# Kernel optimization log

Measured on AMD Instinct MI355X. Metric: run time of the kernel, lower is better.

The kernel has to match this reference:

```python
import jax, jax.numpy as jnp
import numpy as np

B, S, MSL, MQL = 512, 20, 32, 16
E, H, HQ = 32, 32, 32
V, A = 10000, 1000
D = H + S  # per-object feature dim (hidden + one-hot tag) = 52
G = 256


def _lstm_last_h(x, Wih, Whh, bih, bhh):
    # x: [N, T, E]; torch LSTM gate order i,f,g,o; returns final hidden [N, H]
    n, t, _ = x.shape
    h_dim = Whh.shape[1]
    xp = jnp.einsum('nte,ge->ntg', x, Wih) + bih + bhh  # precompute input projection

    def step(carry, xt):
        h, c = carry
        gates = xt + h @ Whh.T
        i, f, g, o = jnp.split(gates, 4, axis=-1)
        c = jax.nn.sigmoid(f) * c + jax.nn.sigmoid(i) * jnp.tanh(g)
        h = jax.nn.sigmoid(o) * jnp.tanh(c)
        return (h, c), None

    init = (jnp.zeros((n, h_dim), x.dtype), jnp.zeros((n, h_dim), x.dtype))
    (h, _), _ = jax.lax.scan(step, init, xp.transpose(1, 0, 2))
    return h


def setup_inputs() -> dict:
    key = jax.random.key(0)
    ks = jax.random.split(key, 24)
    nrm = lambda k, shp, std=0.1: (jax.random.normal(k, shp) * std).astype(jnp.float32)
    inp = {
        'story': jax.random.randint(ks[0], (B, S, MSL), 0, V),
        'question': jax.random.randint(ks[1], (B, MQL), 0, V),
        'emb': nrm(ks[2], (V, E)),
        's_Wih': nrm(ks[3], (4 * H, E)),
        's_Whh': nrm(ks[4], (4 * H, H)),
        's_bih': jnp.zeros((4 * H,), jnp.float32),
        's_bhh': jnp.zeros((4 * H,), jnp.float32),
        'q_Wih': nrm(ks[5], (4 * HQ, E)),
        'q_Whh': nrm(ks[6], (4 * HQ, HQ)),
        'q_bih': jnp.zeros((4 * HQ,), jnp.float32),
        'q_bhh': jnp.zeros((4 * HQ,), jnp.float32),
        'g1_w': nrm(ks[7], (G, 2 * D + HQ)), 'g1_b': jnp.zeros((G,), jnp.float32),
        'g2_w': nrm(ks[8], (G, G)), 'g2_b': jnp.zeros((G,), jnp.float32),
        'g3_w': nrm(ks[9], (G, G)), 'g3_b': jnp.zeros((G,), jnp.float32),
        'g4_w': nrm(ks[10], (G, G)), 'g4_b': jnp.zeros((G,), jnp.float32),
        'f1_w': nrm(ks[11], (G, G)), 'f1_b': jnp.zeros((G,), jnp.float32),
        'f2_w': nrm(ks[12], (512, G)), 'f2_b': jnp.zeros((512,), jnp.float32),
        'f3_w': nrm(ks[13], (A, 512)), 'f3_b': jnp.zeros((A,), jnp.float32),
    }
    return inp


def reference(story, question, emb, s_Wih, s_Whh, s_bih, s_bhh,
              q_Wih, q_Whh, q_bih, q_bhh,
              g1_w, g1_b, g2_w, g2_b, g3_w, g3_b, g4_w, g4_b,
              f1_w, f1_b, f2_w, f2_b, f3_w, f3_b):
    bsz = story.shape[0]
    # story encoding: LSTM over each sentence, take final hidden state
    s_emb = emb[story].reshape(bsz * S, MSL, E)
    s_state = _lstm_last_h(s_emb, s_Wih, s_Whh, s_bih, s_bhh).reshape(bsz, S, H)
    # append one-hot position tags -> story objects [B, S, H+S]
    tags = jnp.broadcast_to(jnp.eye(S, dtype=s_state.dtype), (bsz, S, S))
    obj = jnp.concatenate([s_state, tags], axis=2)
    # question encoding
    q_state = _lstm_last_h(emb[question], q_Wih, q_Whh, q_bih, q_bhh)  # [B, HQ]
    # g_theta over all S*S pairs: g1(cat(o_i, o_j, q)) split into three projections
    Wa, Wb, Wq = g1_w[:, :D], g1_w[:, D:2 * D], g1_w[:, 2 * D:]
    pi = jnp.einsum('bsd,gd->bsg', obj, Wa)   # object-as-first projection
    pj = jnp.einsum('bsd,gd->bsg', obj, Wb)   # object-as-second projection
    pq = q_state @ Wq.T                        # [B, G]
    x = jax.nn.relu(pi[:, :, None, :] + pj[:, None, :, :] + pq[:, None, None, :] + g1_b)  # [B,S,S,G]
    x = jax.nn.relu(jnp.einsum('bijg,hg->bijh', x, g2_w) + g2_b)
    x = jax.nn.relu(jnp.einsum('bijg,hg->bijh', x, g3_w) + g3_b)
    x = jax.nn.relu(jnp.einsum('bijg,hg->bijh', x, g4_w) + g4_b)
    sum_g = x.sum(axis=(1, 2))  # [B, G]
    out = jax.nn.relu(sum_g @ f1_w.T + f1_b)
    out = jax.nn.relu(out @ f2_w.T + f2_b)
    return out @ f3_w.T + f3_b
```

## Files before the change

kernel.cpp:

```cpp
#include <hip/hip_runtime.h>

typedef unsigned short u16;
typedef unsigned int   u32;
typedef __attribute__((ext_vector_type(8))) short short8;
typedef __attribute__((ext_vector_type(4))) float f32x4;

#define OFF_XPS   0
#define OFF_XPQ   1280000
#define OFF_QST   2560000
#define OFF_PI    2576384
#define OFF_PJ    5197824
#define OFF_QA    7819264
#define OFF_TGA   7950336
#define OFF_TGB   7955456
#define OFF_WB    7960576
#define OFF_STB   8058880
#define OFF_WAB   8222720
#define OFF_WBB   8226816
#define OFF_WHHS  8230912
#define OFF_WHHQ  8232960
#define OFF_WF1   8235008
#define OFF_WF2   8267776
#define OFF_WF3   8333312
#define OFF_SGP   0
#define OFF_SGB   655360
#define OFF_ACT1  720896
#define OFF_ACT2  786432

__device__ __forceinline__ u16 f2bf(float f){
  union { float f; u32 u; } v; v.f = f;
  u32 u = v.u;
  u32 r = u + 0x7fffu + ((u >> 16) & 1u);
  return (u16)(r >> 16);
}
__device__ __forceinline__ u32 pack2(float a, float b){
  u32 r;
  asm("v_cvt_pk_bf16_f32 %0, %1, %2" : "=v"(r) : "v"(a), "v"(b));
  return r;
}
__device__ __forceinline__ float sigm(float x){
  return __builtin_amdgcn_rcpf(1.f + __expf(-x));
}

__global__ __launch_bounds__(256) void prep_xp_kernel(
    const float* __restrict__ emb,
    const float* __restrict__ swih, const float* __restrict__ sbih, const float* __restrict__ sbhh,
    const float* __restrict__ qwih, const float* __restrict__ qbih, const float* __restrict__ qbhh,
    float* __restrict__ xps, float* __restrict__ xpq)
{
  __shared__ float wl[4096];
  __shared__ float bl[128];
  const int tid = threadIdx.x;
  const bool isq = blockIdx.y;
  const float* wih = isq ? qwih : swih;
  const float* bih = isq ? qbih : sbih;
  const float* bhh = isq ? qbhh : sbhh;
  float* xp = isq ? xpq : xps;
  #pragma unroll
  for (int k=0;k<16;k++) wl[k*256+tid] = wih[k*256+tid];
  if (tid < 128) bl[tid] = bih[tid] + bhh[tid];
  __syncthreads();
  const int v = blockIdx.x*256 + tid;
  if (v >= 10000) return;
  float4 e[8];
  #pragma unroll
  for (int q=0;q<8;q++) e[q] = *(const float4*)(emb + v*32 + q*4);
  for (int g=0; g<128; ++g){
    float acc = bl[g];
    #pragma unroll
    for (int q=0;q<8;q++){
      float4 w4 = *(const float4*)(&wl[g*32 + q*4]);
      acc = fmaf(e[q].x, w4.x, acc); acc = fmaf(e[q].y, w4.y, acc);
      acc = fmaf(e[q].z, w4.z, acc); acc = fmaf(e[q].w, w4.w, acc);
    }
    xp[v*128 + (g&15)*8 + (g>>4)] = acc;
  }
}

__global__ __launch_bounds__(256) void prep_kernel(
    const float* __restrict__ g2w, const float* __restrict__ g3w, const float* __restrict__ g4w,
    const float* __restrict__ g1w,
    const float* __restrict__ swhh, const float* __restrict__ qwhh,
    const float* __restrict__ f1w, const float* __restrict__ f2w, const float* __restrict__ f3w,
    u16* __restrict__ wb,
    u16* __restrict__ wab, u16* __restrict__ wbb,
    float* __restrict__ tga, float* __restrict__ tgb,
    u16* __restrict__ whhbs, u16* __restrict__ whhbq,
    u16* __restrict__ wf1, u16* __restrict__ wf2, u16* __restrict__ wf3)
{
  const int B = 196608;
  const int C = B + 16384;
  const int D = C + 10240;
  const int E = D + 8192;
  const int F = E + 65536;
  const int G = F + 131072;
  const int H = G + 524288;
  for (int idx = blockIdx.x*256 + threadIdx.x; idx < H; idx += gridDim.x*256){
    if (idx < B){
      const int k = idx;
      const float* src = (k < 65536) ? g2w : ((k < 131072) ? g3w : g4w);
      wb[k] = f2bf(src[k & 65535]);
    } else if (idx < C){
      const int k = idx - B;
      if (k < 8192) wab[k] = f2bf(g1w[(k>>5)*136 + (k&31)]);
      else { const int k2 = k - 8192; wbb[k2] = f2bf(g1w[(k2>>5)*136 + 52 + (k2&31)]); }
    } else if (idx < D){
      const int k = idx - C;
      if (k < 5120){ const int s = k >> 8, g = k & 255; tga[k] = g1w[g*136 + 32 + s]; }
      else { const int k2 = k - 5120; const int s = k2 >> 8, g = k2 & 255; tgb[k2] = g1w[g*136 + 84 + s]; }
    } else if (idx < E){
      const int k = idx - D;
      if (k < 4096) whhbs[k] = f2bf(swhh[k]);
      else whhbq[k-4096] = f2bf(qwhh[k-4096]);
    } else if (idx < F){
      const int k = idx - E;
      wf1[k] = f2bf(f1w[k]);
    } else if (idx < G){
      const int k = idx - F;
      wf2[k] = f2bf(f2w[k]);
    } else {
      const int k = idx - G;
      const int o = k >> 9, kk = k & 511;
      wf3[k] = (o < 1000) ? f2bf(f3w[o*512 + kk]) : (u16)0;
    }
  }
}

template<int LEN>
__device__ __forceinline__ void lstm_mfma_run(
    const int* __restrict__ toks, int s0,
    const float* __restrict__ xpr, const u16* __restrict__ whhb,
    u16* __restrict__ hl, int lane, float* h0r, float* h1r)
{
  const int l15 = lane & 15, l4 = lane >> 4;
  short8 wf[8];
  #pragma unroll
  for (int f=0; f<8; f++)
    wf[f] = *(const short8*)(whhb + (f*16+l15)*32 + l4*8);
  short8 ha = (short8){0,0,0,0,0,0,0,0};
  float c0[4] = {0,0,0,0}, c1[4] = {0,0,0,0};
  int tk[4];
  #pragma unroll
  for (int r=0;r<4;r++) tk[r] = toks[(s0 + l4*4 + r)*LEN];
  float4 xa[4], xb[4];
  #pragma unroll
  for (int r=0;r<4;r++){
    xa[r] = *(const float4*)(xpr + tk[r]*128 + l15*8);
    xb[r] = *(const float4*)(xpr + tk[r]*128 + l15*8 + 4);
  }
  #pragma unroll
  for (int t=0; t<LEN; ++t){
    int tkn[4];
    if (t+1 < LEN){
      #pragma unroll
      for (int r=0;r<4;r++) tkn[r] = toks[(s0 + l4*4 + r)*LEN + t + 1];
    }
    const f32x4 z = (f32x4){0.f,0.f,0.f,0.f};
    f32x4 acc[8];
    #pragma unroll
    for (int f=0; f<8; f++)
      acc[f] = __builtin_amdgcn_mfma_f32_16x16x32_bf16(ha, wf[f], z, 0, 0, 0);
    float4 na[4], nb[4];
    if (t+1 < LEN){
      #pragma unroll
      for (int r=0;r<4;r++){
        na[r] = *(const float4*)(xpr + tkn[r]*128 + l15*8);
        nb[r] = *(const float4*)(xpr + tkn[r]*128 + l15*8 + 4);
      }
    }
    #pragma unroll
    for (int r=0;r<4;r++){
      float i0 = sigm(acc[0][r] + xa[r].x);
      float f0 = sigm(acc[2][r] + xa[r].z);
      float g0 = 2.f*sigm(2.f*(acc[4][r] + xb[r].x)) - 1.f;
      float o0 = sigm(acc[6][r] + xb[r].z);
      c0[r] = fmaf(f0, c0[r], i0*g0);
      h0r[r] = o0 * (2.f*sigm(2.f*c0[r]) - 1.f);
      float i1 = sigm(acc[1][r] + xa[r].y);
      float f1v = sigm(acc[3][r] + xa[r].w);
      float g1v = 2.f*sigm(2.f*(acc[5][r] + xb[r].y)) - 1.f;
      float o1 = sigm(acc[7][r] + xb[r].w);
      c1[r] = fmaf(f1v, c1[r], i1*g1v);
      h1r[r] = o1 * (2.f*sigm(2.f*c1[r]) - 1.f);
    }
    if (t+1 < LEN){
      #pragma unroll
      for (int r=0;r<4;r++){
        hl[(l4*4+r)*32 + l15]      = f2bf(h0r[r]);
        hl[(l4*4+r)*32 + 16 + l15] = f2bf(h1r[r]);
      }
      __syncthreads();
      ha = *(const short8*)(hl + l15*32 + l4*8);
      #pragma unroll
      for (int r=0;r<4;r++){ xa[r] = na[r]; xb[r] = nb[r]; }
    }
  }
}

__global__ __launch_bounds__(64) void lstm_kernel(
    const int* __restrict__ story, const int* __restrict__ question,
    const float* __restrict__ xprs, const float* __restrict__ xprq,
    const u16* __restrict__ whhbs, const u16* __restrict__ whhbq,
    u16* __restrict__ stb, float* __restrict__ qst)
{
  __shared__ u16 hl[512];
  const int lane = threadIdx.x;
  const int w = blockIdx.x;
  const int l15 = lane & 15, l4 = lane >> 4;
  float h0r[4], h1r[4];
  if (w >= 640){
    const int s0 = (w - 640)*16;
    lstm_mfma_run<16>(question, s0, xprq, whhbq, hl, lane, h0r, h1r);
    #pragma unroll
    for (int r=0;r<4;r++){
      qst[(s0 + l4*4 + r)*32 + l15]      = h0r[r];
      qst[(s0 + l4*4 + r)*32 + 16 + l15] = h1r[r];
    }
  } else {
    const int s0 = w*16;
    lstm_mfma_run<32>(story, s0, xprs, whhbs, hl, lane, h0r, h1r);
    #pragma unroll
    for (int r=0;r<4;r++){
      stb[(s0 + l4*4 + r)*32 + l15]      = f2bf(h0r[r]);
      stb[(s0 + l4*4 + r)*32 + 16 + l15] = f2bf(h1r[r]);
    }
  }
}

__global__ __launch_bounds__(256) void pipj_kernel(
    const u16* __restrict__ stb, const u16* __restrict__ wab, const u16* __restrict__ wbb,
    const float* __restrict__ tga, const float* __restrict__ tgb,
    const float* __restrict__ qst, const float* __restrict__ g1w, const float* __restrict__ g1b,
    float* __restrict__ pi, float* __restrict__ pj, float* __restrict__ qa)
{
  const int tid = threadIdx.x;
  if (blockIdx.y == 2){
    for (int idx = blockIdx.x*256 + tid; idx < 131072; idx += 160*256){
      const int b = idx >> 8, g = idx & 255;
      const float* qs = qst + b*32;
      const float* wr = g1w + g*136 + 104;
      float acc = g1b[g];
      #pragma unroll
      for (int q=0;q<8;q++){
        float4 s4 = *(const float4*)(qs + q*4);
        float4 w4 = *(const float4*)(wr + q*4);
        acc = fmaf(s4.x, w4.x, acc); acc = fmaf(s4.y, w4.y, acc);
        acc = fmaf(s4.z, w4.z, acc); acc = fmaf(s4.w, w4.w, acc);
      }
      qa[idx] = acc;
    }
    return;
  }
  const int lane = tid & 63;
  const int wv = tid >> 6;
  const int l15 = lane & 15;
  const int l4 = lane >> 4;
  const int bs0 = blockIdx.x * 64;
  const bool isj = blockIdx.y;
  const u16* wB = isj ? wbb : wab;
  const float* tg = isj ? tgb : tga;
  float* out = isj ? pj : pi;

  short8 af[4], bf[4];
  #pragma unroll
  for (int mf=0; mf<4; mf++)
    af[mf] = *(const short8*)(stb + (bs0 + mf*16 + l15)*32 + l4*8);
  #pragma unroll
  for (int nf=0; nf<4; nf++)
    bf[nf] = *(const short8*)(wB + (wv*64 + nf*16 + l15)*32 + l4*8);

  #pragma unroll
  for (int mf=0; mf<4; mf++){
    #pragma unroll
    for (int nf=0; nf<4; nf++){
      f32x4 acc = (f32x4){0.f,0.f,0.f,0.f};
      acc = __builtin_amdgcn_mfma_f32_16x16x32_bf16(af[mf], bf[nf], acc, 0, 0, 0);
      const int g = wv*64 + nf*16 + l15;
      #pragma unroll
      for (int r=0; r<4; r++){
        const int bs = bs0 + mf*16 + l4*4 + r;
        const int s = bs % 20;
        out[bs*256 + g] = acc[r] + tg[s*256 + g];
      }
    }
  }
}

#define LDX 264
__global__ __launch_bounds__(256) void relnet_kernel(
    const float* __restrict__ pi, const float* __restrict__ pj, const float* __restrict__ qa,
    const u16* __restrict__ w2, const u16* __restrict__ w3, const u16* __restrict__ w4,
    const float* __restrict__ b2, const float* __restrict__ b3, const float* __restrict__ b4,
    float* __restrict__ sgp)
{
  __shared__ u16 Xs[80*LDX];
  const int tid = threadIdx.x;
  const int lane = tid & 63;
  const int wv  = tid >> 6;
  const int b   = blockIdx.x;
  const int t   = blockIdx.y;
  const int l15 = lane & 15;
  const int l4  = lane >> 4;

  const float* pib = pi + b*(20*256);
  const float* pjb = pj + b*(20*256);
  const float* qab = qa + b*256;

  #pragma unroll
  for (int it = 0; it < 10; ++it){
    int u  = it*256 + tid;
    int m  = u >> 5;
    int gq = (u & 31) << 3;
    int R  = t*80 + m;
    int i  = R / 20;
    int j  = R - i*20;
    const float4* pr = (const float4*)(pib + i*256 + gq);
    const float4* qr = (const float4*)(pjb + j*256 + gq);
    const float4* ar = (const float4*)(qab + gq);
    uint4 pk;
    {
      float4 a = pr[0], c4 = qr[0], d4 = ar[0];
      pk.x = pack2(fmaxf(a.x+c4.x+d4.x,0.f), fmaxf(a.y+c4.y+d4.y,0.f));
      pk.y = pack2(fmaxf(a.z+c4.z+d4.z,0.f), fmaxf(a.w+c4.w+d4.w,0.f));
    }
    {
      float4 a = pr[1], c4 = qr[1], d4 = ar[1];
      pk.z = pack2(fmaxf(a.x+c4.x+d4.x,0.f), fmaxf(a.y+c4.y+d4.y,0.f));
      pk.w = pack2(fmaxf(a.z+c4.z+d4.z,0.f), fmaxf(a.w+c4.w+d4.w,0.f));
    }
    *(uint4*)(&Xs[m*LDX + gq]) = pk;
  }
  __syncthreads();

  for (int lay = 0; lay < 2; ++lay){
    const u16*   W    = lay ? w3 : w2;
    const float* bias = lay ? b3 : b2;
    f32x4 acc[4][5];
    #pragma unroll
    for (int hf=0; hf<4; hf++)
      #pragma unroll
      for (int mf=0; mf<5; mf++)
        acc[hf][mf] = (f32x4){0.f,0.f,0.f,0.f};

    #pragma unroll
    for (int kk = 0; kk < 8; ++kk){
      short8 af[4], xf[5];
      #pragma unroll
      for (int hf=0; hf<4; hf++){
        int row = wv*64 + hf*16 + l15;
        af[hf] = *(const short8*)(W + row*256 + kk*32 + l4*8);
      }
      #pragma unroll
      for (int mf=0; mf<5; mf++){
        xf[mf] = *(const short8*)(&Xs[(mf*16 + l15)*LDX + kk*32 + l4*8]);
      }
      #pragma unroll
      for (int hf=0; hf<4; hf++)
        #pragma unroll
        for (int mf=0; mf<5; mf++)
          acc[hf][mf] = __builtin_amdgcn_mfma_f32_16x16x32_bf16(af[hf], xf[mf], acc[hf][mf], 0, 0, 0);
    }

    __syncthreads();
    #pragma unroll
    for (int hf=0; hf<4; hf++){
      int h0 = wv*64 + hf*16 + l4*4;
      float4 bi = *(const float4*)(bias + h0);
      #pragma unroll
      for (int mf=0; mf<5; mf++){
        int m = mf*16 + l15;
        uint2 pk;
        pk.x = pack2(fmaxf(acc[hf][mf][0]+bi.x,0.f), fmaxf(acc[hf][mf][1]+bi.y,0.f));
        pk.y = pack2(fmaxf(acc[hf][mf][2]+bi.z,0.f), fmaxf(acc[hf][mf][3]+bi.w,0.f));
        *(uint2*)(&Xs[m*LDX + h0]) = pk;
      }
    }
    __syncthreads();
  }

  {
    f32x4 acc[4][5];
    #pragma unroll
    for (int hf=0; hf<4; hf++)
      #pragma unroll
      for (int mf=0; mf<5; mf++)
        acc[hf][mf] = (f32x4){0.f,0.f,0.f,0.f};

    #pragma unroll
    for (int kk = 0; kk < 8; ++kk){
      short8 af[4], xf[5];
      #pragma unroll
      for (int hf=0; hf<4; hf++){
        int row = wv*64 + hf*16 + l15;
        af[hf] = *(const short8*)(w4 + row*256 + kk*32 + l4*8);
      }
      #pragma unroll
      for (int mf=0; mf<5; mf++){
        xf[mf] = *(const short8*)(&Xs[(mf*16 + l15)*LDX + kk*32 + l4*8]);
      }
      #pragma unroll
      for (int hf=0; hf<4; hf++)
        #pragma unroll
        for (int mf=0; mf<5; mf++)
          acc[hf][mf] = __builtin_amdgcn_mfma_f32_16x16x32_bf16(af[hf], xf[mf], acc[hf][mf], 0, 0, 0);
    }

    #pragma unroll
    for (int hf=0; hf<4; hf++){
      int h0 = wv*64 + hf*16 + l4*4;
      float4 bi = *(const float4*)(b4 + h0);
      float s0 = 0.f, s1 = 0.f, s2 = 0.f, s3 = 0.f;
      #pragma unroll
      for (int mf=0; mf<5; mf++){
        s0 += fmaxf(acc[hf][mf][0]+bi.x,0.f);
        s1 += fmaxf(acc[hf][mf][1]+bi.y,0.f);
        s2 += fmaxf(acc[hf][mf][2]+bi.z,0.f);
        s3 += fmaxf(acc[hf][mf][3]+bi.w,0.f);
      }
      float sv[4] = {s0, s1, s2, s3};
      #pragma unroll
      for (int r=0; r<4; r++){
        float v = sv[r];
        v += __shfl_xor(v, 1);
        v += __shfl_xor(v, 2);
        v += __shfl_xor(v, 4);
        v += __shfl_xor(v, 8);
        if (l15 == 0){
          int h = h0 + r;
          sgp[t*131072 + h*512 + b] = v;
        }
      }
    }
  }
}

__global__ __launch_bounds__(256) void sgred_kernel(
    const float* __restrict__ sgp, u16* __restrict__ sgb)
{
  const int idx = blockIdx.x*256 + threadIdx.x;
  float v = 0.f;
  #pragma unroll
  for (int t=0;t<5;t++) v += sgp[t*131072 + idx];
  const int g = idx >> 9, b = idx & 511;
  sgb[b*256 + g] = f2bf(v);
}

template<int HF, int KK, int OPAD, int OREAL, int MODE>
__global__ __launch_bounds__(256) void fcm_kernel(
    const u16* __restrict__ in, const u16* __restrict__ w,
    const float* __restrict__ bias, void* __restrict__ outp)
{
  const int K = KK*32;
  const int tid = threadIdx.x, lane = tid & 63, wv = tid >> 6;
  const int l15 = lane & 15, l4 = lane >> 4;
  const int b0 = blockIdx.x*16;
  const int of0 = (blockIdx.y*4 + wv)*HF;
  f32x4 acc[HF];
  #pragma unroll
  for (int hf=0; hf<HF; hf++) acc[hf] = (f32x4){0.f,0.f,0.f,0.f};
  #pragma unroll 4
  for (int kk=0; kk<KK; ++kk){
    short8 xf = *(const short8*)(in + (b0+l15)*K + kk*32 + l4*8);
    #pragma unroll
    for (int hf=0; hf<HF; hf++){
      short8 af = *(const short8*)(w + ((of0+hf)*16 + l15)*K + kk*32 + l4*8);
      acc[hf] = __builtin_amdgcn_mfma_f32_16x16x32_bf16(af, xf, acc[hf], 0, 0, 0);
    }
  }
  const int b = b0 + l15;
  #pragma unroll
  for (int hf=0; hf<HF; hf++){
    const int o0 = (of0+hf)*16 + l4*4;
    float v[4];
    #pragma unroll
    for (int r=0;r<4;r++){
      float bv = (o0+r < OREAL) ? bias[o0+r] : 0.f;
      v[r] = acc[hf][r] + bv;
    }
    if (MODE == 0){
      uint2 pk;
      pk.x = pack2(fmaxf(v[0],0.f), fmaxf(v[1],0.f));
      pk.y = pack2(fmaxf(v[2],0.f), fmaxf(v[3],0.f));
      *(uint2*)((u16*)outp + (size_t)b*OPAD + o0) = pk;
    } else {
      float* of = (float*)outp;
      #pragma unroll
      for (int r=0;r<4;r++)
        if (o0+r < OREAL) of[(size_t)b*OREAL + o0 + r] = v[r];
    }
  }
}

extern "C" void kernel_launch(void* const* d_in, const int* in_sizes, int n_in,
                              void* d_out, int out_size, void* d_ws, size_t ws_size,
                              hipStream_t stream)
{
  const int*   story    = (const int*)d_in[0];
  const int*   question = (const int*)d_in[1];
  const float* emb   = (const float*)d_in[2];
  const float* s_wih = (const float*)d_in[3];
  const float* s_whh = (const float*)d_in[4];
  const float* s_bih = (const float*)d_in[5];
  const float* s_bhh = (const float*)d_in[6];
  const float* q_wih = (const float*)d_in[7];
  const float* q_whh = (const float*)d_in[8];
  const float* q_bih = (const float*)d_in[9];
  const float* q_bhh = (const float*)d_in[10];
  const float* g1w = (const float*)d_in[11];
  const float* g1b = (const float*)d_in[12];
  const float* g2w = (const float*)d_in[13];
  const float* g2b = (const float*)d_in[14];
  const float* g3w = (const float*)d_in[15];
  const float* g3b = (const float*)d_in[16];
  const float* g4w = (const float*)d_in[17];
  const float* g4b = (const float*)d_in[18];
  const float* f1w = (const float*)d_in[19];
  const float* f1b = (const float*)d_in[20];
  const float* f2w = (const float*)d_in[21];
  const float* f2b = (const float*)d_in[22];
  const float* f3w = (const float*)d_in[23];
  const float* f3b = (const float*)d_in[24];

  float* ws  = (float*)d_ws;
  float* xps = ws + OFF_XPS;
  float* xpq = ws + OFF_XPQ;
  float* qst = ws + OFF_QST;
  float* pi  = ws + OFF_PI;
  float* pj  = ws + OFF_PJ;
  float* qa  = ws + OFF_QA;
  float* tga = ws + OFF_TGA;
  float* tgb = ws + OFF_TGB;
  float* sgp = ws + OFF_SGP;
  u16*   wb    = (u16*)(ws + OFF_WB);
  u16*   w2b   = wb;
  u16*   w3b   = wb + 65536;
  u16*   w4b   = wb + 131072;
  u16*   stb   = (u16*)(ws + OFF_STB);
  u16*   wab   = (u16*)(ws + OFF_WAB);
  u16*   wbb   = (u16*)(ws + OFF_WBB);
  u16*   whhbs = (u16*)(ws + OFF_WHHS);
  u16*   whhbq = (u16*)(ws + OFF_WHHQ);
  u16*   wf1   = (u16*)(ws + OFF_WF1);
  u16*   wf2   = (u16*)(ws + OFF_WF2);
  u16*   wf3   = (u16*)(ws + OFF_WF3);
  u16*   sgb   = (u16*)(ws + OFF_SGB);
  u16*   act1  = (u16*)(ws + OFF_ACT1);
  u16*   act2  = (u16*)(ws + OFF_ACT2);

  prep_xp_kernel<<<dim3(40,2), dim3(256), 0, stream>>>(
      emb, s_wih, s_bih, s_bhh, q_wih, q_bih, q_bhh, xps, xpq);
  prep_kernel<<<dim3(1024), dim3(256), 0, stream>>>(
      g2w, g3w, g4w, g1w, s_whh, q_whh, f1w, f2w, f3w,
      wb, wab, wbb, tga, tgb, whhbs, whhbq, wf1, wf2, wf3);
  lstm_kernel<<<dim3(672), dim3(64), 0, stream>>>(
      story, question, xps, xpq, whhbs, whhbq, stb, qst);
  pipj_kernel<<<dim3(160,3), dim3(256), 0, stream>>>(
      stb, wab, wbb, tga, tgb, qst, g1w, g1b, pi, pj, qa);
  relnet_kernel<<<dim3(512,5), dim3(256), 0, stream>>>(
      pi, pj, qa, w2b, w3b, w4b, g2b, g3b, g4b, sgp);
  sgred_kernel<<<dim3(512), dim3(256), 0, stream>>>(sgp, sgb);
  fcm_kernel<1,8,256,256,0><<<dim3(32,4), dim3(256), 0, stream>>>(sgb, wf1, f1b, act1);
  fcm_kernel<2,8,512,512,0><<<dim3(32,4), dim3(256), 0, stream>>>(act1, wf2, f2b, act2);
  fcm_kernel<2,16,1024,1000,1><<<dim3(32,8), dim3(256), 0, stream>>>(act2, wf3, f3b, (float*)d_out);
}
```

Baseline: 235.8 us.

## Fold question projection into pi, prefetch weight fragments, transpose partial-sum layout

```diff
diff --git a/kernel.cpp b/kernel.cpp
--- a/kernel.cpp
+++ b/kernel.cpp
@@ -227,30 +227,32 @@
   }
 }
 
+__global__ __launch_bounds__(256) void qa_kernel(
+    const float* __restrict__ qst, const float* __restrict__ g1w,
+    const float* __restrict__ g1b, float* __restrict__ qa)
+{
+  const int idx = blockIdx.x*256 + threadIdx.x;
+  const int b = idx >> 8, g = idx & 255;
+  const float* qs = qst + b*32;
+  const float* wr = g1w + g*136 + 104;
+  float acc = g1b[g];
+  #pragma unroll
+  for (int q=0;q<8;q++){
+    float4 s4 = *(const float4*)(qs + q*4);
+    float4 w4 = *(const float4*)(wr + q*4);
+    acc = fmaf(s4.x, w4.x, acc); acc = fmaf(s4.y, w4.y, acc);
+    acc = fmaf(s4.z, w4.z, acc); acc = fmaf(s4.w, w4.w, acc);
+  }
+  qa[idx] = acc;
+}
+
 __global__ __launch_bounds__(256) void pipj_kernel(
     const u16* __restrict__ stb, const u16* __restrict__ wab, const u16* __restrict__ wbb,
     const float* __restrict__ tga, const float* __restrict__ tgb,
-    const float* __restrict__ qst, const float* __restrict__ g1w, const float* __restrict__ g1b,
-    float* __restrict__ pi, float* __restrict__ pj, float* __restrict__ qa)
+    const float* __restrict__ qa,
+    float* __restrict__ pi, float* __restrict__ pj)
 {
   const int tid = threadIdx.x;
-  if (blockIdx.y == 2){
-    for (int idx = blockIdx.x*256 + tid; idx < 131072; idx += 160*256){
-      const int b = idx >> 8, g = idx & 255;
-      const float* qs = qst + b*32;
-      const float* wr = g1w + g*136 + 104;
-      float acc = g1b[g];
-      #pragma unroll
-      for (int q=0;q<8;q++){
-        float4 s4 = *(const float4*)(qs + q*4);
-        float4 w4 = *(const float4*)(wr + q*4);
-        acc = fmaf(s4.x, w4.x, acc); acc = fmaf(s4.y, w4.y, acc);
-        acc = fmaf(s4.z, w4.z, acc); acc = fmaf(s4.w, w4.w, acc);
-      }
-      qa[idx] = acc;
-    }
-    return;
-  }
   const int lane = tid & 63;
   const int wv = tid >> 6;
   const int l15 = lane & 15;
@@ -280,7 +282,9 @@
       for (int r=0; r<4; r++){
         const int bs = bs0 + mf*16 + l4*4 + r;
         const int s = bs % 20;
-        out[bs*256 + g] = acc[r] + tg[s*256 + g];
+        float v = acc[r] + tg[s*256 + g];
+        if (!isj) v += qa[(bs/20)*256 + g];
+        out[bs*256 + g] = v;
       }
     }
   }
@@ -288,7 +292,7 @@
 
 #define LDX 264
 __global__ __launch_bounds__(256) void relnet_kernel(
-    const float* __restrict__ pi, const float* __restrict__ pj, const float* __restrict__ qa,
+    const float* __restrict__ pi, const float* __restrict__ pj,
     const u16* __restrict__ w2, const u16* __restrict__ w3, const u16* __restrict__ w4,
     const float* __restrict__ b2, const float* __restrict__ b3, const float* __restrict__ b4,
     float* __restrict__ sgp)
@@ -304,7 +308,6 @@
 
   const float* pib = pi + b*(20*256);
   const float* pjb = pj + b*(20*256);
-  const float* qab = qa + b*256;
 
   #pragma unroll
   for (int it = 0; it < 10; ++it){
@@ -316,21 +319,22 @@
     int j  = R - i*20;
     const float4* pr = (const float4*)(pib + i*256 + gq);
     const float4* qr = (const float4*)(pjb + j*256 + gq);
-    const float4* ar = (const float4*)(qab + gq);
     uint4 pk;
     {
-      float4 a = pr[0], c4 = qr[0], d4 = ar[0];
-      pk.x = pack2(fmaxf(a.x+c4.x+d4.x,0.f), fmaxf(a.y+c4.y+d4.y,0.f));
-      pk.y = pack2(fmaxf(a.z+c4.z+d4.z,0.f), fmaxf(a.w+c4.w+d4.w,0.f));
+      float4 a = pr[0], c4 = qr[0];
+      pk.x = pack2(fmaxf(a.x+c4.x,0.f), fmaxf(a.y+c4.y,0.f));
+      pk.y = pack2(fmaxf(a.z+c4.z,0.f), fmaxf(a.w+c4.w,0.f));
     }
     {
-      float4 a = pr[1], c4 = qr[1], d4 = ar[1];
-      pk.z = pack2(fmaxf(a.x+c4.x+d4.x,0.f), fmaxf(a.y+c4.y+d4.y,0.f));
-      pk.w = pack2(fmaxf(a.z+c4.z+d4.z,0.f), fmaxf(a.w+c4.w+d4.w,0.f));
+      float4 a = pr[1], c4 = qr[1];
+      pk.z = pack2(fmaxf(a.x+c4.x,0.f), fmaxf(a.y+c4.y,0.f));
+      pk.w = pack2(fmaxf(a.z+c4.z,0.f), fmaxf(a.w+c4.w,0.f));
     }
     *(uint4*)(&Xs[m*LDX + gq]) = pk;
   }
   __syncthreads();
+
+  const int arow = wv*64 + l15;
 
   for (int lay = 0; lay < 2; ++lay){
     const u16*   W    = lay ? w3 : w2;
@@ -342,23 +346,28 @@
       for (int mf=0; mf<5; mf++)
         acc[hf][mf] = (f32x4){0.f,0.f,0.f,0.f};
 
+    short8 af0[4], af1[4];
+    #pragma unroll
+    for (int hf=0; hf<4; hf++)
+      af0[hf] = *(const short8*)(W + (arow + hf*16)*256 + l4*8);
+
     #pragma unroll
     for (int kk = 0; kk < 8; ++kk){
-      short8 af[4], xf[5];
-      #pragma unroll
-      for (int hf=0; hf<4; hf++){
-        int row = wv*64 + hf*16 + l15;
-        af[hf] = *(const short8*)(W + row*256 + kk*32 + l4*8);
-      }
-      #pragma unroll
-      for (int mf=0; mf<5; mf++){
+      const int kn = (kk < 7) ? kk+1 : 7;
+      #pragma unroll
+      for (int hf=0; hf<4; hf++)
+        af1[hf] = *(const short8*)(W + (arow + hf*16)*256 + kn*32 + l4*8);
+      short8 xf[5];
+      #pragma unroll
+      for (int mf=0; mf<5; mf++)
         xf[mf] = *(const short8*)(&Xs[(mf*16 + l15)*LDX + kk*32 + l4*8]);
-      }
       #pragma unroll
       for (int hf=0; hf<4; hf++)
         #pragma unroll
         for (int mf=0; mf<5; mf++)
-          acc[hf][mf] = __builtin_amdgcn_mfma_f32_16x16x32_bf16(af[hf], xf[mf], acc[hf][mf], 0, 0, 0);
+          acc[hf][mf] = __builtin_amdgcn_mfma_f32_16x16x32_bf16(af0[hf], xf[mf], acc[hf][mf], 0, 0, 0);
+      #pragma unroll
+      for (int hf=0; hf<4; hf++) af0[hf] = af1[hf];
     }
 
     __syncthreads();
@@ -386,23 +395,28 @@
       for (int mf=0; mf<5; mf++)
         acc[hf][mf] = (f32x4){0.f,0.f,0.f,0.f};
 
+    short8 af0[4], af1[4];
+    #pragma unroll
+    for (int hf=0; hf<4; hf++)
+      af0[hf] = *(const short8*)(w4 + (arow + hf*16)*256 + l4*8);
+
     #pragma unroll
     for (int kk = 0; kk < 8; ++kk){
-      short8 af[4], xf[5];
-      #pragma unroll
-      for (int hf=0; hf<4; hf++){
-        int row = wv*64 + hf*16 + l15;
-        af[hf] = *(const short8*)(w4 + row*256 + kk*32 + l4*8);
-      }
-      #pragma unroll
-      for (int mf=0; mf<5; mf++){
+      const int kn = (kk < 7) ? kk+1 : 7;
+      #pragma unroll
+      for (int hf=0; hf<4; hf++)
+        af1[hf] = *(const short8*)(w4 + (arow + hf*16)*256 + kn*32 + l4*8);
+      short8 xf[5];
+      #pragma unroll
+      for (int mf=0; mf<5; mf++)
         xf[mf] = *(const short8*)(&Xs[(mf*16 + l15)*LDX + kk*32 + l4*8]);
-      }
       #pragma unroll
       for (int hf=0; hf<4; hf++)
         #pragma unroll
         for (int mf=0; mf<5; mf++)
-          acc[hf][mf] = __builtin_amdgcn_mfma_f32_16x16x32_bf16(af[hf], xf[mf], acc[hf][mf], 0, 0, 0);
+          acc[hf][mf] = __builtin_amdgcn_mfma_f32_16x16x32_bf16(af0[hf], xf[mf], acc[hf][mf], 0, 0, 0);
+      #pragma unroll
+      for (int hf=0; hf<4; hf++) af0[hf] = af1[hf];
     }
 
     #pragma unroll
@@ -427,7 +441,7 @@
         v += __shfl_xor(v, 8);
         if (l15 == 0){
           int h = h0 + r;
-          sgp[t*131072 + h*512 + b] = v;
+          sgp[t*131072 + b*256 + h] = v;
         }
       }
     }
@@ -441,8 +455,7 @@
   float v = 0.f;
   #pragma unroll
   for (int t=0;t<5;t++) v += sgp[t*131072 + idx];
-  const int g = idx >> 9, b = idx & 511;
-  sgb[b*256 + g] = f2bf(v);
+  sgb[idx] = f2bf(v);
 }
 
 template<int HF, int KK, int OPAD, int OREAL, int MODE>
@@ -554,10 +567,11 @@
       wb, wab, wbb, tga, tgb, whhbs, whhbq, wf1, wf2, wf3);
   lstm_kernel<<<dim3(672), dim3(64), 0, stream>>>(
       story, question, xps, xpq, whhbs, whhbq, stb, qst);
-  pipj_kernel<<<dim3(160,3), dim3(256), 0, stream>>>(
-      stb, wab, wbb, tga, tgb, qst, g1w, g1b, pi, pj, qa);
+  qa_kernel<<<dim3(512), dim3(256), 0, stream>>>(qst, g1w, g1b, qa);
+  pipj_kernel<<<dim3(160,2), dim3(256), 0, stream>>>(
+      stb, wab, wbb, tga, tgb, qa, pi, pj);
   relnet_kernel<<<dim3(512,5), dim3(256), 0, stream>>>(
-      pi, pj, qa, w2b, w3b, w4b, g2b, g3b, g4b, sgp);
+      pi, pj, w2b, w3b, w4b, g2b, g3b, g4b, sgp);
   sgred_kernel<<<dim3(512), dim3(256), 0, stream>>>(sgp, sgb);
   fcm_kernel<1,8,256,256,0><<<dim3(32,4), dim3(256), 0, stream>>>(sgb, wf1, f1b, act1);
   fcm_kernel<2,8,512,512,0><<<dim3(32,4), dim3(256), 0, stream>>>(act1, wf2, f2b, act2);
```

Result: slower. 249.2 us (+5.7%).
